# Kernel tuning notes

Measured on AMD Instinct MI355X. Metric: run time of the kernel, lower is better.

## Reference

```python
import jax, jax.numpy as jnp
import numpy as np

T, D_MODEL, D_FF, N_EXPERTS, TOPK = 4096, 2048, 8192, 8, 2


def setup_inputs() -> dict:
    key = jax.random.key(0)
    k1, k2, k3, k4 = jax.random.split(key, 4)
    x = jax.random.normal(k1, (T, D_MODEL), dtype=jnp.float32)
    gating_output = jax.random.normal(k2, (T, N_EXPERTS), dtype=jnp.float32)
    # gate_proj and up_proj concatenated along output dim: [E, 2*d_ff, d_model]
    gate_up_proj = jax.random.normal(k3, (N_EXPERTS, 2 * D_FF, D_MODEL), dtype=jnp.float32) * 0.02
    # down_proj: [E, d_model, d_ff]
    down_proj = jax.random.normal(k4, (N_EXPERTS, D_MODEL, D_FF), dtype=jnp.float32) * 0.02
    return {"x": x, "gating_output": gating_output, "gate_up_proj": gate_up_proj,
            "down_proj": down_proj, "topk": TOPK}


def reference(x, gating_output, gate_up_proj, down_proj, topk):
    n_experts = gate_up_proj.shape[0]
    d_ff = down_proj.shape[2]
    # Router: fp32 softmax over experts, top-k, renormalize over the k selected.
    probs = jax.nn.softmax(gating_output.astype(jnp.float32), axis=1)  # [T, E]
    routing_weights, selected_experts = jax.lax.top_k(probs, topk)     # [T, k]
    routing_weights = routing_weights / jnp.sum(routing_weights, axis=-1, keepdims=True)
    routing_weights = routing_weights.astype(x.dtype)
    # Expert MLPs: silu(x @ Wg^T) * (x @ Wu^T) @ Wd^T, combined by routing weight.
    out = jnp.zeros_like(x)
    for e in range(n_experts):  # small fixed expert count
        coef = jnp.sum(jnp.where(selected_experts == e, routing_weights, 0.0), axis=-1)  # [T]
        gu = x @ gate_up_proj[e].T                     # [T, 2*d_ff]
        h = jax.nn.silu(gu[:, :d_ff]) * gu[:, d_ff:]   # [T, d_ff]
        out = out + coef[:, None] * (h @ down_proj[e].T)  # [T, d_model]
    return out
```

## Files before the change

kernel.cpp:

```cpp
#include <hip/hip_runtime.h>
#include <hip/hip_bf16.h>
#include <cstdint>
#include <cstddef>

#define T_TOK 4096
#define DMODEL 2048
#define DFF 8192
#define NEXP 8
#define NPAIR (T_TOK * 2)

typedef __bf16 bf16_t;
typedef __bf16 bf16x8 __attribute__((ext_vector_type(8)));
typedef float fx4 __attribute__((ext_vector_type(4)));

__device__ __forceinline__ void gload16(const bf16_t* src, bf16_t* dst) {
    __builtin_amdgcn_global_load_lds(
        (const __attribute__((address_space(1))) uint32_t*)(src),
        (__attribute__((address_space(3))) uint32_t*)(dst), 16, 0, 0);
}

__device__ __forceinline__ bf16x8 pack8(const fx4 lo, const fx4 hi) {
    bf16x8 o;
    o[0] = (bf16_t)lo[0]; o[1] = (bf16_t)lo[1]; o[2] = (bf16_t)lo[2]; o[3] = (bf16_t)lo[3];
    o[4] = (bf16_t)hi[0]; o[5] = (bf16_t)hi[1]; o[6] = (bf16_t)hi[2]; o[7] = (bf16_t)hi[3];
    return o;
}

__global__ void router_kernel(const float* __restrict__ gating, int* __restrict__ counts,
                              int* __restrict__ tok_list, float* __restrict__ w_list) {
    int t = blockIdx.x * blockDim.x + threadIdx.x;
    if (t >= T_TOK) return;
    float l[NEXP];
    float mx = -1e30f;
#pragma unroll
    for (int e = 0; e < NEXP; e++) { l[e] = gating[t * NEXP + e]; mx = fmaxf(mx, l[e]); }
#pragma unroll
    for (int e = 0; e < NEXP; e++) { l[e] = __expf(l[e] - mx); }
    int e0 = 0; float p0 = l[0];
#pragma unroll
    for (int e = 1; e < NEXP; e++) { if (l[e] > p0) { p0 = l[e]; e0 = e; } }
    int e1 = -1; float p1 = -1.0f;
#pragma unroll
    for (int e = 0; e < NEXP; e++) { if (e != e0 && l[e] > p1) { p1 = l[e]; e1 = e; } }
    float inv = 1.0f / (p0 + p1);
    int s0 = atomicAdd(&counts[e0], 1);
    tok_list[e0 * T_TOK + s0] = t; w_list[e0 * T_TOK + s0] = p0 * inv;
    int s1 = atomicAdd(&counts[e1], 1);
    tok_list[e1 * T_TOK + s1] = t; w_list[e1 * T_TOK + s1] = p1 * inv;
}

__global__ void scan_kernel(const int* __restrict__ counts, int* __restrict__ offsets) {
    if (threadIdx.x == 0 && blockIdx.x == 0) {
        int acc = 0;
        for (int e = 0; e < NEXP; e++) { offsets[e] = acc; acc += counts[e]; }
        offsets[NEXP] = acc;
    }
}

__global__ void cvt_x_kernel(const float* __restrict__ x, bf16_t* __restrict__ xb) {
    int i = blockIdx.x * blockDim.x + threadIdx.x;
    const fx4* src = (const fx4*)x;
    fx4 v0 = src[2 * i], v1 = src[2 * i + 1];
    *(bf16x8*)(xb + (size_t)i * 8) = pack8(v0, v1);
}

__global__ __launch_bounds__(256, 3) void gateup_kernel(
    const bf16_t* __restrict__ xb, const float* __restrict__ gup,
    const int* __restrict__ counts, const int* __restrict__ offsets,
    const int* __restrict__ tok_list, bf16_t* __restrict__ h_buf)
{
    const int e = blockIdx.y;
    const int cnt = counts[e];
    const int s = blockIdx.x;
    const int mbase = ((s >> 3) & 31) * 128;
    if (mbase >= cnt) return;
    const int y = (s & 7) + 8 * (s >> 8);
    const int nbase = y * 64;
    const int off_e = offsets[e];

    __shared__ __align__(16) bf16_t lds_a[128 * 64];
    __shared__ __align__(16) bf16_t lds_w[128 * 64];

    const int tid = threadIdx.x;
    const int lane = tid & 63;
    const int w = tid >> 6;
    const int wm = (w >> 1) * 64;
    const int wn = (w & 1) * 32;

    const bf16_t* a_src[4];
    bf16_t* a_dst[4];
#pragma unroll
    for (int j = 0; j < 4; j++) {
        int sidx = (w * 4 + j) * 64 + lane;
        int row = sidx >> 3;
        int cc = (lane & 7) ^ (row & 7);
        int slot = mbase + row;
        int tok = (slot < cnt) ? tok_list[e * T_TOK + slot] : 0;
        a_src[j] = xb + (size_t)tok * DMODEL + cc * 8;
        a_dst[j] = lds_a + (w * 4 + j) * 512;
    }
    const float* w_src[4];
    int w_st[4];
    const float* gbase = gup + (size_t)e * (2 * DFF) * DMODEL;
#pragma unroll
    for (int t = 0; t < 4; t++) {
        int cid = t * 256 + tid;
        int row = cid >> 3, c = cid & 7;
        int grow = (row < 64) ? (nbase + row) : (DFF + nbase + (row - 64));
        w_src[t] = gbase + (size_t)grow * DMODEL + c * 8;
        w_st[t] = row * 64 + ((c ^ (row & 7)) * 8);
    }

    fx4 accg[4][2] = {};
    fx4 accu[4][2] = {};

    for (int k0 = 0; k0 < DMODEL; k0 += 64) {
#pragma unroll
        for (int j = 0; j < 4; j++) { gload16(a_src[j], a_dst[j]); a_src[j] += 64; }
#pragma unroll
        for (int t = 0; t < 4; t++) {
            fx4 lo = *(const fx4*)(w_src[t]);
            fx4 hi = *(const fx4*)(w_src[t] + 4);
            w_src[t] += 64;
            *(bf16x8*)(&lds_w[w_st[t]]) = pack8(lo, hi);
        }
        __syncthreads();
#pragma unroll
        for (int kp = 0; kp < 2; kp++) {
            const int ke = kp * 4 + (lane >> 4);
            bf16x8 af[4], gf[2], uf[2];
#pragma unroll
            for (int i = 0; i < 4; i++) {
                int row = wm + i * 16 + (lane & 15);
                af[i] = *(const bf16x8*)(&lds_a[row * 64 + ((ke ^ (row & 7)) * 8)]);
            }
#pragma unroll
            for (int n = 0; n < 2; n++) {
                int row = wn + n * 16 + (lane & 15);
                gf[n] = *(const bf16x8*)(&lds_w[row * 64 + ((ke ^ (row & 7)) * 8)]);
                uf[n] = *(const bf16x8*)(&lds_w[(row + 64) * 64 + ((ke ^ (row & 7)) * 8)]);
            }
#pragma unroll
            for (int i = 0; i < 4; i++)
#pragma unroll
                for (int n = 0; n < 2; n++) {
                    accg[i][n] = __builtin_amdgcn_mfma_f32_16x16x32_bf16(af[i], gf[n], accg[i][n], 0, 0, 0);
                    accu[i][n] = __builtin_amdgcn_mfma_f32_16x16x32_bf16(af[i], uf[n], accu[i][n], 0, 0, 0);
                }
        }
        __syncthreads();
    }

    const int colbase = nbase + wn + (lane & 15);
#pragma unroll
    for (int i = 0; i < 4; i++) {
        int rbase = wm + i * 16 + ((lane >> 4) * 4);
#pragma unroll
        for (int j = 0; j < 4; j++) {
            int slot = mbase + rbase + j;
            if (slot < cnt) {
                size_t hrow = (size_t)(off_e + slot);
#pragma unroll
                for (int n = 0; n < 2; n++) {
                    float g = accg[i][n][j];
                    float u = accu[i][n][j];
                    float hv = g * u / (1.0f + __expf(-g));
                    h_buf[hrow * DFF + colbase + n * 16] = (bf16_t)hv;
                }
            }
        }
    }
}

__global__ __launch_bounds__(256, 3) void down_kernel(
    const bf16_t* __restrict__ h_buf, const float* __restrict__ dwn,
    const int* __restrict__ counts, const int* __restrict__ offsets,
    const int* __restrict__ tok_list, const float* __restrict__ w_list,
    float* __restrict__ out)
{
    const int e = blockIdx.y;
    const int cnt = counts[e];
    const int s = blockIdx.x;
    const int mbase = ((s >> 3) & 31) * 128;
    if (mbase >= cnt) return;
    const int y = (s & 7) + 8 * (s >> 8);
    const int nbase = y * 128;
    const int off_e = offsets[e];

    __shared__ __align__(16) bf16_t lds_a[128 * 64];
    __shared__ __align__(16) bf16_t lds_b[128 * 64];

    const int tid = threadIdx.x;
    const int lane = tid & 63;
    const int w = tid >> 6;
    const int wm = (w >> 1) * 64;
    const int wn = (w & 1) * 64;

    const bf16_t* a_src[4];
    bf16_t* a_dst[4];
#pragma unroll
    for (int j = 0; j < 4; j++) {
        int sidx = (w * 4 + j) * 64 + lane;
        int row = sidx >> 3;
        int cc = (lane & 7) ^ (row & 7);
        int hrow = off_e + mbase + row;
        if (hrow > NPAIR - 1) hrow = NPAIR - 1;
        a_src[j] = h_buf + (size_t)hrow * DFF + cc * 8;
        a_dst[j] = lds_a + (w * 4 + j) * 512;
    }
    const float* b_src[4];
    int b_st[4];
    const float* bbase = dwn + (size_t)e * DMODEL * DFF;
#pragma unroll
    for (int t = 0; t < 4; t++) {
        int cid = t * 256 + tid;
        int row = cid >> 3, c = cid & 7;
        b_src[t] = bbase + (size_t)(nbase + row) * DFF + c * 8;
        b_st[t] = row * 64 + ((c ^ (row & 7)) * 8);
    }

    fx4 acc[4][4] = {};

    for (int k0 = 0; k0 < DFF; k0 += 64) {
#pragma unroll
        for (int j = 0; j < 4; j++) { gload16(a_src[j], a_dst[j]); a_src[j] += 64; }
#pragma unroll
        for (int t = 0; t < 4; t++) {
            fx4 lo = *(const fx4*)(b_src[t]);
            fx4 hi = *(const fx4*)(b_src[t] + 4);
            b_src[t] += 64;
            *(bf16x8*)(&lds_b[b_st[t]]) = pack8(lo, hi);
        }
        __syncthreads();
#pragma unroll
        for (int kp = 0; kp < 2; kp++) {
            const int ke = kp * 4 + (lane >> 4);
            bf16x8 af[4], bfr[4];
#pragma unroll
            for (int i = 0; i < 4; i++) {
                int row = wm + i * 16 + (lane & 15);
                af[i] = *(const bf16x8*)(&lds_a[row * 64 + ((ke ^ (row & 7)) * 8)]);
            }
#pragma unroll
            for (int n = 0; n < 4; n++) {
                int row = wn + n * 16 + (lane & 15);
                bfr[n] = *(const bf16x8*)(&lds_b[row * 64 + ((ke ^ (row & 7)) * 8)]);
            }
#pragma unroll
            for (int i = 0; i < 4; i++)
#pragma unroll
                for (int n = 0; n < 4; n++)
                    acc[i][n] = __builtin_amdgcn_mfma_f32_16x16x32_bf16(af[i], bfr[n], acc[i][n], 0, 0, 0);
        }
        __syncthreads();
    }

    const int colbase = nbase + wn + (lane & 15);
#pragma unroll
    for (int i = 0; i < 4; i++) {
        int rbase = wm + i * 16 + ((lane >> 4) * 4);
#pragma unroll
        for (int j = 0; j < 4; j++) {
            int slot = mbase + rbase + j;
            if (slot < cnt) {
                int tok = tok_list[e * T_TOK + slot];
                float wgt = w_list[e * T_TOK + slot];
#pragma unroll
                for (int n = 0; n < 4; n++)
                    atomicAdd(&out[(size_t)tok * DMODEL + colbase + n * 16], wgt * acc[i][n][j]);
            }
        }
    }
}

extern "C" void kernel_launch(void* const* d_in, const int* in_sizes, int n_in,
                              void* d_out, int out_size, void* d_ws, size_t ws_size,
                              hipStream_t stream) {
    const float* x      = (const float*)d_in[0];
    const float* gating = (const float*)d_in[1];
    const float* gup    = (const float*)d_in[2];
    const float* dwn    = (const float*)d_in[3];
    float* out = (float*)d_out;

    char* ws = (char*)d_ws;
    int*    counts   = (int*)(ws + 0);
    int*    offsets  = (int*)(ws + 64);
    int*    tok_list = (int*)(ws + 128);
    float*  w_list   = (float*)(ws + 128 + 131072);
    bf16_t* xb       = (bf16_t*)(ws + 262400);
    bf16_t* h_buf    = (bf16_t*)(ws + 17039872);

    hipMemsetAsync(counts, 0, 64, stream);
    hipMemsetAsync(out, 0, (size_t)out_size * sizeof(float), stream);

    router_kernel<<<dim3(T_TOK / 256), dim3(256), 0, stream>>>(gating, counts, tok_list, w_list);
    scan_kernel<<<dim3(1), dim3(64), 0, stream>>>(counts, offsets);
    cvt_x_kernel<<<dim3(T_TOK * DMODEL / 8 / 256), dim3(256), 0, stream>>>(x, xb);

    gateup_kernel<<<dim3(4096, NEXP), dim3(256), 0, stream>>>(
        xb, gup, counts, offsets, tok_list, h_buf);

    down_kernel<<<dim3(512, NEXP), dim3(256), 0, stream>>>(
        h_buf, dwn, counts, offsets, tok_list, w_list, out);
}
```

Baseline: 1.599 ms.

## Double-buffer LDS with register prefetch and enlarge MoE GEMM tiles

Both expert GEMM kernels move to 512-thread blocks with 256-row M tiles and wider N tiles, so each block computes more output per weight and activation load. Shared memory is double-buffered: the next K-slice of fp32 weights is prefetched into registers and the activation slice is loaded asynchronously into the other buffer while MFMAs run on the current one. Explicit waitcnt, raw barriers and s_setprio replace the two __syncthreads per step. The cost is more registers, 128 KB of LDS per block and lower occupancy, and the hand-placed wait counts must match the number of outstanding loads.

```diff
diff --git a/kernel.cpp b/kernel.cpp
--- a/kernel.cpp
+++ b/kernel.cpp
@@ -64,106 +64,131 @@
     *(bf16x8*)(xb + (size_t)i * 8) = pack8(v0, v1);
 }
 
-__global__ __launch_bounds__(256, 3) void gateup_kernel(
+#define GU_NT (DMODEL / 64)
+
+__global__ __launch_bounds__(512, 2) void gateup_kernel(
     const bf16_t* __restrict__ xb, const float* __restrict__ gup,
     const int* __restrict__ counts, const int* __restrict__ offsets,
     const int* __restrict__ tok_list, bf16_t* __restrict__ h_buf)
 {
-    const int e = blockIdx.y;
+    const int idx = blockIdx.x;
+    const int q = idx & 7;
+    const int rest = idx >> 3;
+    const int mslot = rest & 15;
+    const int g2 = rest >> 4;
+    const int e = g2 >> 3;
     const int cnt = counts[e];
-    const int s = blockIdx.x;
-    const int mbase = ((s >> 3) & 31) * 128;
+    const int mbase = mslot * 256;
     if (mbase >= cnt) return;
-    const int y = (s & 7) + 8 * (s >> 8);
-    const int nbase = y * 64;
+    const int y = q + 8 * (g2 & 7);
+    const int nbase = y * 128;
     const int off_e = offsets[e];
 
-    __shared__ __align__(16) bf16_t lds_a[128 * 64];
-    __shared__ __align__(16) bf16_t lds_w[128 * 64];
+    __shared__ __align__(16) bf16_t lds_a[2][256 * 64];
+    __shared__ __align__(16) bf16_t lds_w[2][256 * 64];
 
     const int tid = threadIdx.x;
     const int lane = tid & 63;
     const int w = tid >> 6;
     const int wm = (w >> 1) * 64;
-    const int wn = (w & 1) * 32;
+    const int wnh = (w & 1) * 64;
 
     const bf16_t* a_src[4];
-    bf16_t* a_dst[4];
+    int a_dstoff[4];
 #pragma unroll
     for (int j = 0; j < 4; j++) {
-        int sidx = (w * 4 + j) * 64 + lane;
-        int row = sidx >> 3;
-        int cc = (lane & 7) ^ (row & 7);
+        int row = (w * 4 + j) * 8 + (lane >> 3);
+        int cs = (lane & 7) ^ (row & 7);
         int slot = mbase + row;
-        int tok = (slot < cnt) ? tok_list[e * T_TOK + slot] : 0;
-        a_src[j] = xb + (size_t)tok * DMODEL + cc * 8;
-        a_dst[j] = lds_a + (w * 4 + j) * 512;
-    }
-    const float* w_src[4];
-    int w_st[4];
-    const float* gbase = gup + (size_t)e * (2 * DFF) * DMODEL;
-#pragma unroll
-    for (int t = 0; t < 4; t++) {
-        int cid = t * 256 + tid;
-        int row = cid >> 3, c = cid & 7;
-        int grow = (row < 64) ? (nbase + row) : (DFF + nbase + (row - 64));
-        w_src[t] = gbase + (size_t)grow * DMODEL + c * 8;
-        w_st[t] = row * 64 + ((c ^ (row & 7)) * 8);
-    }
-
-    fx4 accg[4][2] = {};
-    fx4 accu[4][2] = {};
-
-    for (int k0 = 0; k0 < DMODEL; k0 += 64) {
-#pragma unroll
-        for (int j = 0; j < 4; j++) { gload16(a_src[j], a_dst[j]); a_src[j] += 64; }
-#pragma unroll
-        for (int t = 0; t < 4; t++) {
-            fx4 lo = *(const fx4*)(w_src[t]);
-            fx4 hi = *(const fx4*)(w_src[t] + 4);
-            w_src[t] += 64;
-            *(bf16x8*)(&lds_w[w_st[t]]) = pack8(lo, hi);
-        }
-        __syncthreads();
+        int tok = tok_list[e * T_TOK + (slot < cnt ? slot : cnt - 1)];
+        a_src[j] = xb + (size_t)tok * DMODEL + cs * 8;
+        a_dstoff[j] = (w * 4 + j) * 512;
+    }
+    const int wrow = tid >> 1;
+    const int whalf = tid & 1;
+    const int grow = (wrow < 128) ? (nbase + wrow) : (DFF + nbase + (wrow - 128));
+    const float* w_src = gup + (size_t)e * (2 * DFF) * DMODEL + (size_t)grow * DMODEL + whalf * 32;
+    int w_doff[4];
+#pragma unroll
+    for (int c4 = 0; c4 < 4; c4++) {
+        int c = whalf * 4 + c4;
+        w_doff[c4] = wrow * 64 + ((c ^ (wrow & 7)) * 8);
+    }
+
+    fx4 accg[4][4] = {};
+    fx4 accu[4][4] = {};
+    fx4 wreg[8];
+
+#pragma unroll
+    for (int i = 0; i < 8; i++) wreg[i] = *(const fx4*)(w_src + i * 4);
+#pragma unroll
+    for (int j = 0; j < 4; j++) gload16(a_src[j], &lds_a[0][a_dstoff[j]]);
+
+    for (int t = 0; t < GU_NT; ++t) {
+        const int cur = t & 1;
+        asm volatile("s_waitcnt vmcnt(4)" ::: "memory");
+        bf16_t* wb = lds_w[cur];
+#pragma unroll
+        for (int c4 = 0; c4 < 4; c4++)
+            *(bf16x8*)(&wb[w_doff[c4]]) = pack8(wreg[c4 * 2], wreg[c4 * 2 + 1]);
+        if (t + 1 < GU_NT) {
+            const float* ws = w_src + (t + 1) * 64;
+#pragma unroll
+            for (int i = 0; i < 8; i++) wreg[i] = *(const fx4*)(ws + i * 4);
+#pragma unroll
+            for (int j = 0; j < 4; j++)
+                gload16(a_src[j] + (t + 1) * 64, &lds_a[cur ^ 1][a_dstoff[j]]);
+            asm volatile("s_waitcnt vmcnt(12) lgkmcnt(0)" ::: "memory");
+        } else {
+            asm volatile("s_waitcnt vmcnt(0) lgkmcnt(0)" ::: "memory");
+        }
+        __builtin_amdgcn_s_barrier();
+        asm volatile("" ::: "memory");
+
+        const bf16_t* A = lds_a[cur];
+        const bf16_t* W = lds_w[cur];
+        __builtin_amdgcn_s_setprio(1);
 #pragma unroll
         for (int kp = 0; kp < 2; kp++) {
             const int ke = kp * 4 + (lane >> 4);
-            bf16x8 af[4], gf[2], uf[2];
-#pragma unroll
-            for (int i = 0; i < 4; i++) {
-                int row = wm + i * 16 + (lane & 15);
-                af[i] = *(const bf16x8*)(&lds_a[row * 64 + ((ke ^ (row & 7)) * 8)]);
-            }
-#pragma unroll
-            for (int n = 0; n < 2; n++) {
-                int row = wn + n * 16 + (lane & 15);
-                gf[n] = *(const bf16x8*)(&lds_w[row * 64 + ((ke ^ (row & 7)) * 8)]);
-                uf[n] = *(const bf16x8*)(&lds_w[(row + 64) * 64 + ((ke ^ (row & 7)) * 8)]);
-            }
-#pragma unroll
-            for (int i = 0; i < 4; i++)
-#pragma unroll
-                for (int n = 0; n < 2; n++) {
-                    accg[i][n] = __builtin_amdgcn_mfma_f32_16x16x32_bf16(af[i], gf[n], accg[i][n], 0, 0, 0);
-                    accu[i][n] = __builtin_amdgcn_mfma_f32_16x16x32_bf16(af[i], uf[n], accu[i][n], 0, 0, 0);
+            bf16x8 af[4], gf[4], uf[4];
+#pragma unroll
+            for (int m = 0; m < 4; m++) {
+                int r = wm + m * 16 + (lane & 15);
+                af[m] = *(const bf16x8*)(&A[r * 64 + ((ke ^ (r & 7)) * 8)]);
+            }
+#pragma unroll
+            for (int n = 0; n < 4; n++) {
+                int r = wnh + n * 16 + (lane & 15);
+                gf[n] = *(const bf16x8*)(&W[r * 64 + ((ke ^ (r & 7)) * 8)]);
+                uf[n] = *(const bf16x8*)(&W[(r + 128) * 64 + ((ke ^ (r & 7)) * 8)]);
+            }
+#pragma unroll
+            for (int m = 0; m < 4; m++)
+#pragma unroll
+                for (int n = 0; n < 4; n++) {
+                    accg[m][n] = __builtin_amdgcn_mfma_f32_16x16x32_bf16(af[m], gf[n], accg[m][n], 0, 0, 0);
+                    accu[m][n] = __builtin_amdgcn_mfma_f32_16x16x32_bf16(af[m], uf[n], accu[m][n], 0, 0, 0);
                 }
         }
-        __syncthreads();
-    }
-
-    const int colbase = nbase + wn + (lane & 15);
-#pragma unroll
-    for (int i = 0; i < 4; i++) {
-        int rbase = wm + i * 16 + ((lane >> 4) * 4);
+        __builtin_amdgcn_s_setprio(0);
+        asm volatile("" ::: "memory");
+        __builtin_amdgcn_s_barrier();
+    }
+
+    const int colbase = nbase + wnh + (lane & 15);
+#pragma unroll
+    for (int m = 0; m < 4; m++) {
+        int rb = wm + m * 16 + ((lane >> 4) * 4);
 #pragma unroll
         for (int j = 0; j < 4; j++) {
-            int slot = mbase + rbase + j;
+            int slot = mbase + rb + j;
             if (slot < cnt) {
                 size_t hrow = (size_t)(off_e + slot);
 #pragma unroll
-                for (int n = 0; n < 2; n++) {
-                    float g = accg[i][n][j];
-                    float u = accu[i][n][j];
+                for (int n = 0; n < 4; n++) {
+                    float g = accg[m][n][j];
+                    float u = accu[m][n][j];
                     float hv = g * u / (1.0f + __expf(-g));
                     h_buf[hrow * DFF + colbase + n * 16] = (bf16_t)hv;
                 }
@@ -172,102 +197,125 @@
     }
 }
 
-__global__ __launch_bounds__(256, 3) void down_kernel(
+#define DN_NT (DFF / 64)
+
+__global__ __launch_bounds__(512, 2) void down_kernel(
     const bf16_t* __restrict__ h_buf, const float* __restrict__ dwn,
     const int* __restrict__ counts, const int* __restrict__ offsets,
     const int* __restrict__ tok_list, const float* __restrict__ w_list,
     float* __restrict__ out)
 {
-    const int e = blockIdx.y;
+    const int idx = blockIdx.x;
+    const int y = idx & 7;
+    const int rest = idx >> 3;
+    const int mslot = rest & 15;
+    const int e = rest >> 4;
     const int cnt = counts[e];
-    const int s = blockIdx.x;
-    const int mbase = ((s >> 3) & 31) * 128;
+    const int mbase = mslot * 256;
     if (mbase >= cnt) return;
-    const int y = (s & 7) + 8 * (s >> 8);
-    const int nbase = y * 128;
+    const int nbase = y * 256;
     const int off_e = offsets[e];
 
-    __shared__ __align__(16) bf16_t lds_a[128 * 64];
-    __shared__ __align__(16) bf16_t lds_b[128 * 64];
+    __shared__ __align__(16) bf16_t lds_a[2][256 * 64];
+    __shared__ __align__(16) bf16_t lds_w[2][256 * 64];
 
     const int tid = threadIdx.x;
     const int lane = tid & 63;
     const int w = tid >> 6;
     const int wm = (w >> 1) * 64;
-    const int wn = (w & 1) * 64;
+    const int wn = (w & 1) * 128;
 
     const bf16_t* a_src[4];
-    bf16_t* a_dst[4];
+    int a_dstoff[4];
 #pragma unroll
     for (int j = 0; j < 4; j++) {
-        int sidx = (w * 4 + j) * 64 + lane;
-        int row = sidx >> 3;
-        int cc = (lane & 7) ^ (row & 7);
-        int hrow = off_e + mbase + row;
-        if (hrow > NPAIR - 1) hrow = NPAIR - 1;
-        a_src[j] = h_buf + (size_t)hrow * DFF + cc * 8;
-        a_dst[j] = lds_a + (w * 4 + j) * 512;
-    }
-    const float* b_src[4];
-    int b_st[4];
-    const float* bbase = dwn + (size_t)e * DMODEL * DFF;
-#pragma unroll
-    for (int t = 0; t < 4; t++) {
-        int cid = t * 256 + tid;
-        int row = cid >> 3, c = cid & 7;
-        b_src[t] = bbase + (size_t)(nbase + row) * DFF + c * 8;
-        b_st[t] = row * 64 + ((c ^ (row & 7)) * 8);
-    }
-
-    fx4 acc[4][4] = {};
-
-    for (int k0 = 0; k0 < DFF; k0 += 64) {
-#pragma unroll
-        for (int j = 0; j < 4; j++) { gload16(a_src[j], a_dst[j]); a_src[j] += 64; }
-#pragma unroll
-        for (int t = 0; t < 4; t++) {
-            fx4 lo = *(const fx4*)(b_src[t]);
-            fx4 hi = *(const fx4*)(b_src[t] + 4);
-            b_src[t] += 64;
-            *(bf16x8*)(&lds_b[b_st[t]]) = pack8(lo, hi);
-        }
-        __syncthreads();
+        int row = (w * 4 + j) * 8 + (lane >> 3);
+        int cs = (lane & 7) ^ (row & 7);
+        int slot = mbase + row;
+        int hrow = off_e + (slot < cnt ? slot : cnt - 1);
+        a_src[j] = h_buf + (size_t)hrow * DFF + cs * 8;
+        a_dstoff[j] = (w * 4 + j) * 512;
+    }
+    const int wrow = tid >> 1;
+    const int whalf = tid & 1;
+    const float* w_src = dwn + (size_t)e * DMODEL * DFF + (size_t)(nbase + wrow) * DFF + whalf * 32;
+    int w_doff[4];
+#pragma unroll
+    for (int c4 = 0; c4 < 4; c4++) {
+        int c = whalf * 4 + c4;
+        w_doff[c4] = wrow * 64 + ((c ^ (wrow & 7)) * 8);
+    }
+
+    fx4 acc[4][8] = {};
+    fx4 wreg[8];
+
+#pragma unroll
+    for (int i = 0; i < 8; i++) wreg[i] = *(const fx4*)(w_src + i * 4);
+#pragma unroll
+    for (int j = 0; j < 4; j++) gload16(a_src[j], &lds_a[0][a_dstoff[j]]);
+
+    for (int t = 0; t < DN_NT; ++t) {
+        const int cur = t & 1;
+        asm volatile("s_waitcnt vmcnt(4)" ::: "memory");
+        bf16_t* wb = lds_w[cur];
+#pragma unroll
+        for (int c4 = 0; c4 < 4; c4++)
+            *(bf16x8*)(&wb[w_doff[c4]]) = pack8(wreg[c4 * 2], wreg[c4 * 2 + 1]);
+        if (t + 1 < DN_NT) {
+            const float* ws = w_src + (t + 1) * 64;
+#pragma unroll
+            for (int i = 0; i < 8; i++) wreg[i] = *(const fx4*)(ws + i * 4);
+#pragma unroll
+            for (int j = 0; j < 4; j++)
+                gload16(a_src[j] + (t + 1) * 64, &lds_a[cur ^ 1][a_dstoff[j]]);
+            asm volatile("s_waitcnt vmcnt(12) lgkmcnt(0)" ::: "memory");
+        } else {
+            asm volatile("s_waitcnt vmcnt(0) lgkmcnt(0)" ::: "memory");
+        }
+        __builtin_amdgcn_s_barrier();
+        asm volatile("" ::: "memory");
+
+        const bf16_t* A = lds_a[cur];
+        const bf16_t* W = lds_w[cur];
+        __builtin_amdgcn_s_setprio(1);
 #pragma unroll
         for (int kp = 0; kp < 2; kp++) {
             const int ke = kp * 4 + (lane >> 4);
-            bf16x8 af[4], bfr[4];
-#pragma unroll
-            for (int i = 0; i < 4; i++) {
-                int row = wm + i * 16 + (lane & 15);
-                af[i] = *(const bf16x8*)(&lds_a[row * 64 + ((ke ^ (row & 7)) * 8)]);
-            }
-#pragma unroll
-            for (int n = 0; n < 4; n++) {
-                int row = wn + n * 16 + (lane & 15);
-                bfr[n] = *(const bf16x8*)(&lds_b[row * 64 + ((ke ^ (row & 7)) * 8)]);
-            }
-#pragma unroll
-            for (int i = 0; i < 4; i++)
-#pragma unroll
-                for (int n = 0; n < 4; n++)
-                    acc[i][n] = __builtin_amdgcn_mfma_f32_16x16x32_bf16(af[i], bfr[n], acc[i][n], 0, 0, 0);
-        }
-        __syncthreads();
-    }
-
-    const int colbase = nbase + wn + (lane & 15);
-#pragma unroll
-    for (int i = 0; i < 4; i++) {
-        int rbase = wm + i * 16 + ((lane >> 4) * 4);
+            bf16x8 af[4], bf[8];
+#pragma unroll
+            for (int m = 0; m < 4; m++) {
+                int r = wm + m * 16 + (lane & 15);
+                af[m] = *(const bf16x8*)(&A[r * 64 + ((ke ^ (r & 7)) * 8)]);
+            }
+#pragma unroll
+            for (int n = 0; n < 8; n++) {
+                int r = wn + n * 16 + (lane & 15);
+                bf[n] = *(const bf16x8*)(&W[r * 64 + ((ke ^ (r & 7)) * 8)]);
+            }
+#pragma unroll
+            for (int m = 0; m < 4; m++)
+#pragma unroll
+                for (int n = 0; n < 8; n++)
+                    acc[m][n] = __builtin_amdgcn_mfma_f32_16x16x32_bf16(af[m], bf[n], acc[m][n], 0, 0, 0);
+        }
+        __builtin_amdgcn_s_setprio(0);
+        asm volatile("" ::: "memory");
+        __builtin_amdgcn_s_barrier();
+    }
+
+    const int colb = nbase + wn + (lane & 15);
+#pragma unroll
+    for (int m = 0; m < 4; m++) {
+        int rb = wm + m * 16 + ((lane >> 4) * 4);
 #pragma unroll
         for (int j = 0; j < 4; j++) {
-            int slot = mbase + rbase + j;
+            int slot = mbase + rb + j;
             if (slot < cnt) {
                 int tok = tok_list[e * T_TOK + slot];
                 float wgt = w_list[e * T_TOK + slot];
 #pragma unroll
-                for (int n = 0; n < 4; n++)
-                    atomicAdd(&out[(size_t)tok * DMODEL + colbase + n * 16], wgt * acc[i][n][j]);
+                for (int n = 0; n < 8; n++)
+                    atomicAdd(&out[(size_t)tok * DMODEL + colb + n * 16], wgt * acc[m][n][j]);
             }
         }
     }
@@ -297,9 +345,9 @@
     scan_kernel<<<dim3(1), dim3(64), 0, stream>>>(counts, offsets);
     cvt_x_kernel<<<dim3(T_TOK * DMODEL / 8 / 256), dim3(256), 0, stream>>>(x, xb);
 
-    gateup_kernel<<<dim3(4096, NEXP), dim3(256), 0, stream>>>(
+    gateup_kernel<<<dim3(8192), dim3(512), 0, stream>>>(
         xb, gup, counts, offsets, tok_list, h_buf);
 
-    down_kernel<<<dim3(512, NEXP), dim3(256), 0, stream>>>(
+    down_kernel<<<dim3(1024), dim3(512), 0, stream>>>(
         h_buf, dwn, counts, offsets, tok_list, w_list, out);
 }
```

New measurement: 2.546 ms. 59.2% more time.
